# Optimization experiments

Hardware: AMD Instinct MI355X
Metric: run time of the kernel (lower is better)

The kernel has to match this reference:

```python
import jax, jax.numpy as jnp
import numpy as np

N_NODES = 100000
N_EDGES = 800000
VOCAB = 100
D_FEAT = 10
D = 64
EPS = 1e-8  # torch F.cosine_similarity eps


def setup_inputs() -> dict:
    key = jax.random.key(0)
    ks = jax.random.split(key, 8)
    return {
        "nodes": jax.random.randint(ks[0], (N_NODES,), 0, VOCAB),
        "edges": jax.random.randint(ks[1], (N_EDGES, 2), 0, N_NODES),
        "features": jax.random.normal(ks[2], (N_NODES, D_FEAT), dtype=jnp.float32),
        "node_emb": jax.random.normal(ks[3], (VOCAB, D), dtype=jnp.float32),
        "feat_W": jax.random.normal(ks[4], (D, D_FEAT), dtype=jnp.float32) * 0.1,
        "feat_b": jnp.zeros((D,), dtype=jnp.float32),
        "conv1_W": jax.random.normal(ks[5], (D, D), dtype=jnp.float32) * 0.1,
        "conv1_b": jnp.zeros((D,), dtype=jnp.float32),
        "pattern_emb": jax.random.normal(ks[6], (VOCAB, D), dtype=jnp.float32),
        "pattern_id": 42,  # hash(node_type) % 100
    }


def reference(nodes, edges, features, node_emb, feat_W, feat_b,
              conv1_W, conv1_b, pattern_emb, pattern_id):
    # initial embeddings: type embedding + linear feature projection  [N, D]
    embeds = node_emb[nodes] + (features @ feat_W.T + feat_b)

    src, dst = edges[:, 0], edges[:, 1]
    for _ in range(2):  # fixed 2 message-passing rounds (structural loop)
        # scatter-add messages from src to dst (order-independent sum)
        agg = jnp.zeros_like(embeds).at[dst].add(embeds[src])
        embeds = jax.nn.relu((embeds + agg) @ conv1_W.T + conv1_b)

    # cosine similarity of each node embedding against the pattern embedding
    p = pattern_emb[pattern_id]  # [D]
    num = embeds @ p  # [N]
    denom = jnp.maximum(jnp.linalg.norm(embeds, axis=1), EPS) * \
            jnp.maximum(jnp.linalg.norm(p), EPS)
    return num / denom  # [N] match scores
```

## Files before the change

kernel.cpp:

```cpp
#include <hip/hip_runtime.h>
#include <hip/hip_bf16.h>

#define N_NODES 100000
#define N_EDGES 800000
#define D 64
#define SCAN_B 256
#define NB1 ((N_NODES + SCAN_B - 1) / SCAN_B)
#define FILL_BLOCKS (N_EDGES / 256)
#define INIT_BLOCKS (N_NODES * D / 256)

__device__ __forceinline__ unsigned short f2bf(float f) {
    union { float f; unsigned u; } v; v.f = f;
    unsigned r = v.u + 0x7fffu + ((v.u >> 16) & 1u);
    return (unsigned short)(r >> 16);
}
__device__ __forceinline__ void acc_bf8(float acc[8], uint4 u) {
    acc[0] += __uint_as_float(u.x << 16);
    acc[1] += __uint_as_float(u.x & 0xffff0000u);
    acc[2] += __uint_as_float(u.y << 16);
    acc[3] += __uint_as_float(u.y & 0xffff0000u);
    acc[4] += __uint_as_float(u.z << 16);
    acc[5] += __uint_as_float(u.z & 0xffff0000u);
    acc[6] += __uint_as_float(u.w << 16);
    acc[7] += __uint_as_float(u.w & 0xffff0000u);
}

__global__ __launch_bounds__(256) void hist_rank_kernel(
        const int2* __restrict__ edges,
        int* __restrict__ deg,
        int* __restrict__ rank) {
    int t = blockIdx.x * 256 + threadIdx.x;
    int2 e = edges[t];
    rank[t] = atomicAdd(&deg[e.y], 1);
}

__global__ void scan1_kernel(const int* __restrict__ deg,
                             int* __restrict__ row_ptr,
                             int* __restrict__ bsum) {
    __shared__ int tmp[SCAN_B];
    int t = threadIdx.x;
    int i = blockIdx.x * SCAN_B + t;
    int v = (i < N_NODES) ? deg[i] : 0;
    tmp[t] = v;
    __syncthreads();
#pragma unroll
    for (int off = 1; off < SCAN_B; off <<= 1) {
        int a = (t >= off) ? tmp[t - off] : 0;
        __syncthreads();
        tmp[t] += a;
        __syncthreads();
    }
    if (i < N_NODES) row_ptr[i] = tmp[t] - v;
    if (t == SCAN_B - 1) bsum[blockIdx.x] = tmp[t];
}

__global__ void scan2_kernel(const int* __restrict__ bsum, int* __restrict__ boff) {
    __shared__ int tmp[512];
    int t = threadIdx.x;
    int v = (t < NB1) ? bsum[t] : 0;
    tmp[t] = v;
    __syncthreads();
#pragma unroll
    for (int off = 1; off < 512; off <<= 1) {
        int a = (t >= off) ? tmp[t - off] : 0;
        __syncthreads();
        tmp[t] += a;
        __syncthreads();
    }
    if (t < NB1) boff[t] = tmp[t] - v;
}

__global__ void scan3_kernel(int* __restrict__ row_ptr,
                             const int* __restrict__ boff) {
    int i = blockIdx.x * SCAN_B + threadIdx.x;
    if (i < N_NODES) row_ptr[i] += boff[i >> 8];
    if (i == 0) row_ptr[N_NODES] = N_EDGES;
}

__global__ __launch_bounds__(256) void fill_init_kernel(
        const int2* __restrict__ edges,
        const int* __restrict__ rank,
        const int* __restrict__ rowp,
        int* __restrict__ col,
        const int* __restrict__ nodes,
        const float* __restrict__ features,
        const float* __restrict__ node_emb,
        const float* __restrict__ feat_W,
        const float* __restrict__ feat_b,
        unsigned short* __restrict__ embeds) {
    if (blockIdx.x < FILL_BLOCKS) {
        int t = blockIdx.x * 256 + threadIdx.x;
        int2 e = edges[t];
        col[rowp[e.y] + rank[t]] = e.x;
    } else {
        int tid = (blockIdx.x - FILL_BLOCKS) * 256 + threadIdx.x;
        int node = tid >> 6;
        int d = tid & 63;
        float acc = feat_b[d];
        const float* f = features + (size_t)node * 10;
        const float* w = feat_W + (size_t)d * 10;
#pragma unroll
        for (int j = 0; j < 10; ++j) acc += f[j] * w[j];
        embeds[tid] = f2bf(node_emb[(size_t)nodes[node] * D + d] + acc);
    }
}

__global__ __launch_bounds__(256, 6) void gather_x_kernel(
        const unsigned short* __restrict__ emb_in,
        const int* __restrict__ rowp,
        const int* __restrict__ col,
        float* __restrict__ x_out) {
    int lane = threadIdx.x & 63;
    int wv   = threadIdx.x >> 6;
    int node = blockIdx.x * 4 + wv;
    int g = lane >> 3;
    int c = lane & 7;

    int start = rowp[node];
    int end   = rowp[node + 1];

    float acc[8];
#pragma unroll
    for (int j = 0; j < 8; ++j) acc[j] = 0.f;
    if (g == 0) {
        uint4 u = ((const uint4*)(emb_in + (size_t)node * D))[c];
        acc_bf8(acc, u);
    }

    for (int base = start; base < end; base += 32) {
        int nb = end - base; if (nb > 32) nb = 32;
        int idx = (lane < nb) ? col[base + lane] : 0;
#pragma unroll
        for (int r = 0; r < 4; ++r) {
            int s = r * 8 + g;
            int src = __shfl(idx, s, 64);
            if (s < nb) {
                uint4 u = ((const uint4*)(emb_in + (size_t)src * D))[c];
                acc_bf8(acc, u);
            }
        }
    }

#pragma unroll
    for (int m = 8; m <= 32; m <<= 1) {
#pragma unroll
        for (int j = 0; j < 8; ++j) acc[j] += __shfl_xor(acc[j], m, 64);
    }

    if (g == 0) {
        float4 a0 = make_float4(acc[0], acc[1], acc[2], acc[3]);
        float4 a1 = make_float4(acc[4], acc[5], acc[6], acc[7]);
        float4* o = (float4*)(x_out + (size_t)node * D);
        o[2 * c]     = a0;
        o[2 * c + 1] = a1;
    }
}

template <bool SCORE>
__global__ __launch_bounds__(256) void conv_kernel(
        const float* __restrict__ x,
        const float* __restrict__ W,
        const float* __restrict__ b,
        const float* __restrict__ pattern_emb,
        const int* __restrict__ pattern_id,
        unsigned short* __restrict__ emb_out,
        float* __restrict__ score_out) {
    __shared__ float4 xs[4][16];

    int lane = threadIdx.x & 63;
    int wv   = threadIdx.x >> 6;
    float bias = b[lane];

    float4 Wr[16];
    const float4* W4 = (const float4*)(W + (size_t)lane * D);
#pragma unroll
    for (int k = 0; k < 16; ++k) Wr[k] = W4[k];

    float p = 0.f, pnorm = 1.f;
    if (SCORE) {
        p = pattern_emb[(size_t)pattern_id[0] * D + lane];
        float pn = p * p;
#pragma unroll
        for (int m = 32; m > 0; m >>= 1) pn += __shfl_xor(pn, m, 64);
        pnorm = fmaxf(sqrtf(pn), 1e-8f);
    }

    const int n_chunks = N_NODES / 4;
    for (int chunk = blockIdx.x; chunk < n_chunks; chunk += gridDim.x) {
        int node = chunk * 4 + wv;
        if (lane < 16)
            xs[wv][lane] = ((const float4*)(x + (size_t)node * D))[lane];
        asm volatile("s_waitcnt vmcnt(0) lgkmcnt(0)" ::: "memory");
        float y = bias;
#pragma unroll
        for (int k = 0; k < 16; ++k) {
            float4 x4 = xs[wv][k];
            y += Wr[k].x * x4.x + Wr[k].y * x4.y + Wr[k].z * x4.z + Wr[k].w * x4.w;
        }
        y = fmaxf(y, 0.0f);
        if (!SCORE) {
            emb_out[(size_t)node * D + lane] = f2bf(y);
        } else {
            float dot = y * p;
            float n2  = y * y;
#pragma unroll
            for (int m = 32; m > 0; m >>= 1) {
                dot += __shfl_xor(dot, m, 64);
                n2  += __shfl_xor(n2, m, 64);
            }
            if (lane == 0)
                score_out[node] = dot / (fmaxf(sqrtf(n2), 1e-8f) * pnorm);
        }
    }
}

__global__ void init_embeds_kernel(const int* __restrict__ nodes,
                                   const float* __restrict__ features,
                                   const float* __restrict__ node_emb,
                                   const float* __restrict__ feat_W,
                                   const float* __restrict__ feat_b,
                                   float* __restrict__ embeds) {
    int tid = blockIdx.x * blockDim.x + threadIdx.x;
    if (tid >= N_NODES * D) return;
    int node = tid >> 6;
    int d = tid & 63;
    float acc = feat_b[d];
    const float* f = features + (size_t)node * 10;
    const float* w = feat_W + (size_t)d * 10;
#pragma unroll
    for (int j = 0; j < 10; ++j) acc += f[j] * w[j];
    embeds[tid] = node_emb[(size_t)nodes[node] * D + d] + acc;
}

__global__ void scatter_add_kernel(const int* __restrict__ edges,
                                   const float* __restrict__ embeds,
                                   float* __restrict__ agg) {
    int tid = blockIdx.x * blockDim.x + threadIdx.x;
    int edge = tid >> 6;
    int lane = tid & 63;
    if (edge >= N_EDGES) return;
    int src = edges[2 * edge + 0];
    int dst = edges[2 * edge + 1];
    atomicAdd(&agg[(size_t)dst * D + lane], embeds[(size_t)src * D + lane]);
}

__global__ void conv_inplace_kernel(const float* __restrict__ agg,
                                    const float* __restrict__ W,
                                    const float* __restrict__ b,
                                    float* __restrict__ embeds) {
    __shared__ float Ws[D * 65];
    __shared__ float xs[4][D];
    for (int i = threadIdx.x; i < D * D; i += blockDim.x) {
        int d = i >> 6, k = i & 63;
        Ws[d * 65 + k] = W[i];
    }
    __syncthreads();
    int lane_d = threadIdx.x & 63;
    int local_n = threadIdx.x >> 6;
    float bias = b[lane_d];
    const int n_chunks = (N_NODES + 3) / 4;
    for (int chunk = blockIdx.x; chunk < n_chunks; chunk += gridDim.x) {
        int node = chunk * 4 + local_n;
        if (node < N_NODES) {
            size_t base = (size_t)node * D + lane_d;
            xs[local_n][lane_d] = embeds[base] + agg[base];
        }
        __syncthreads();
        if (node < N_NODES) {
            float acc = bias;
#pragma unroll
            for (int k = 0; k < D; ++k) acc += xs[local_n][k] * Ws[lane_d * 65 + k];
            embeds[(size_t)node * D + lane_d] = fmaxf(acc, 0.0f);
        }
        __syncthreads();
    }
}

__global__ void final_score_kernel(const float* __restrict__ embeds,
                                   const float* __restrict__ pattern_emb,
                                   const int* __restrict__ pattern_id,
                                   float* __restrict__ out) {
    int lane = threadIdx.x & 63;
    int wave = threadIdx.x >> 6;
    int node = blockIdx.x * 4 + wave;
    int pid = pattern_id[0];
    float p = pattern_emb[(size_t)pid * D + lane];
    float pn = p * p;
#pragma unroll
    for (int m = 32; m > 0; m >>= 1) pn += __shfl_xor(pn, m, 64);
    if (node < N_NODES) {
        float e = embeds[(size_t)node * D + lane];
        float dot = e * p;
        float n2 = e * e;
#pragma unroll
        for (int m = 32; m > 0; m >>= 1) {
            dot += __shfl_xor(dot, m, 64);
            n2  += __shfl_xor(n2, m, 64);
        }
        if (lane == 0) {
            float denom = fmaxf(sqrtf(n2), 1e-8f) * fmaxf(sqrtf(pn), 1e-8f);
            out[node] = dot / denom;
        }
    }
}

extern "C" void kernel_launch(void* const* d_in, const int* in_sizes, int n_in,
                              void* d_out, int out_size, void* d_ws, size_t ws_size,
                              hipStream_t stream) {
    const int*   nodes       = (const int*)d_in[0];
    const int*   edges       = (const int*)d_in[1];
    const float* features    = (const float*)d_in[2];
    const float* node_emb    = (const float*)d_in[3];
    const float* feat_W      = (const float*)d_in[4];
    const float* feat_b      = (const float*)d_in[5];
    const float* conv1_W     = (const float*)d_in[6];
    const float* conv1_b     = (const float*)d_in[7];
    const float* pattern_emb = (const float*)d_in[8];
    const int*   pattern_id  = (const int*)d_in[9];
    float* out = (float*)d_out;

    const size_t emb_f32_bytes = (size_t)N_NODES * D * sizeof(float);
    const size_t emb_bf_bytes  = (size_t)N_NODES * D * 2;
    auto align256 = [](size_t x) { return (x + 255) & ~(size_t)255; };

    size_t o_embA = 0;
    size_t o_embB = o_embA + align256(emb_bf_bytes);
    size_t o_xbuf = o_embB + align256(emb_bf_bytes);
    size_t o_col  = o_xbuf + align256(emb_f32_bytes);
    size_t o_rank = o_col  + align256((size_t)N_EDGES * 4);
    size_t o_row  = o_rank + align256((size_t)N_EDGES * 4);
    size_t o_deg  = o_row  + align256((size_t)(N_NODES + 1) * 4);
    size_t o_bsum = o_deg  + align256((size_t)N_NODES * 4);
    size_t o_boff = o_bsum + align256((size_t)NB1 * 4);
    size_t need   = o_boff + align256((size_t)NB1 * 4);

    char* ws = (char*)d_ws;

    if (ws_size >= need) {
        unsigned short* embA = (unsigned short*)(ws + o_embA);
        unsigned short* embB = (unsigned short*)(ws + o_embB);
        float* xbuf = (float*)(ws + o_xbuf);
        int*   col  = (int*)(ws + o_col);
        int*   rank = (int*)(ws + o_rank);
        int*   rowp = (int*)(ws + o_row);
        int*   deg  = (int*)(ws + o_deg);
        int*   bsum = (int*)(ws + o_bsum);
        int*   boff = (int*)(ws + o_boff);

        hipMemsetAsync(deg, 0, (size_t)N_NODES * 4, stream);
        hist_rank_kernel<<<FILL_BLOCKS, 256, 0, stream>>>((const int2*)edges, deg, rank);
        scan1_kernel<<<NB1, SCAN_B, 0, stream>>>(deg, rowp, bsum);
        scan2_kernel<<<1, 512, 0, stream>>>(bsum, boff);
        scan3_kernel<<<NB1, SCAN_B, 0, stream>>>(rowp, boff);
        fill_init_kernel<<<FILL_BLOCKS + INIT_BLOCKS, 256, 0, stream>>>(
            (const int2*)edges, rank, rowp, col,
            nodes, features, node_emb, feat_W, feat_b, embA);

        gather_x_kernel<<<N_NODES / 4, 256, 0, stream>>>(embA, rowp, col, xbuf);
        conv_kernel<false><<<2048, 256, 0, stream>>>(
            xbuf, conv1_W, conv1_b, pattern_emb, pattern_id, embB, nullptr);
        gather_x_kernel<<<N_NODES / 4, 256, 0, stream>>>(embB, rowp, col, xbuf);
        conv_kernel<true><<<2048, 256, 0, stream>>>(
            xbuf, conv1_W, conv1_b, pattern_emb, pattern_id, nullptr, out);
    } else {
        float* embeds = (float*)ws;
        float* agg = (float*)(ws + align256(emb_f32_bytes));
        init_embeds_kernel<<<(N_NODES * D + 255) / 256, 256, 0, stream>>>(
            nodes, features, node_emb, feat_W, feat_b, embeds);
        for (int it = 0; it < 2; ++it) {
            hipMemsetAsync(agg, 0, emb_f32_bytes, stream);
            long long total = (long long)N_EDGES * 64;
            scatter_add_kernel<<<(int)((total + 255) / 256), 256, 0, stream>>>(edges, embeds, agg);
            conv_inplace_kernel<<<2048, 256, 0, stream>>>(agg, conv1_W, conv1_b, embeds);
        }
        final_score_kernel<<<(N_NODES + 3) / 4, 256, 0, stream>>>(
            embeds, pattern_emb, pattern_id, out);
    }
}
```

Baseline: 300.6 us.

## Replace per-node conv GEMV with 64-node shared-memory tiled GEMM

The dense conv step now processes 64 nodes per block as a small tiled GEMM. X and W are staged in padded shared memory and each thread computes a 4x4 output register tile. It drops the old grid-stride loop, where each wave held a full W row in registers and stalled on a full memory wait per node. Outputs are staged in shared memory for coalesced 16-byte bf16 stores, and the score path reduces each node's dot product and norm in one thread. This trades per-block W reloads and extra barriers for more arithmetic reuse and far more blocks in flight.

After: 259.7 us. 1.16x faster.

```diff
diff --git a/kernel.cpp b/kernel.cpp
--- a/kernel.cpp
+++ b/kernel.cpp
@@ -8,6 +8,9 @@
 #define NB1 ((N_NODES + SCAN_B - 1) / SCAN_B)
 #define FILL_BLOCKS (N_EDGES / 256)
 #define INIT_BLOCKS (N_NODES * D / 256)
+#define CT 64
+#define XS 68
+#define OS 72
 
 __device__ __forceinline__ unsigned short f2bf(float f) {
     union { float f; unsigned u; } v; v.f = f;
@@ -157,7 +160,7 @@
 }
 
 template <bool SCORE>
-__global__ __launch_bounds__(256) void conv_kernel(
+__global__ __launch_bounds__(256) void conv_tile_kernel(
         const float* __restrict__ x,
         const float* __restrict__ W,
         const float* __restrict__ b,
@@ -165,51 +168,86 @@
         const int* __restrict__ pattern_id,
         unsigned short* __restrict__ emb_out,
         float* __restrict__ score_out) {
-    __shared__ float4 xs[4][16];
-
-    int lane = threadIdx.x & 63;
-    int wv   = threadIdx.x >> 6;
-    float bias = b[lane];
-
-    float4 Wr[16];
-    const float4* W4 = (const float4*)(W + (size_t)lane * D);
-#pragma unroll
-    for (int k = 0; k < 16; ++k) Wr[k] = W4[k];
-
-    float p = 0.f, pnorm = 1.f;
-    if (SCORE) {
-        p = pattern_emb[(size_t)pattern_id[0] * D + lane];
-        float pn = p * p;
-#pragma unroll
-        for (int m = 32; m > 0; m >>= 1) pn += __shfl_xor(pn, m, 64);
-        pnorm = fmaxf(sqrtf(pn), 1e-8f);
-    }
-
-    const int n_chunks = N_NODES / 4;
-    for (int chunk = blockIdx.x; chunk < n_chunks; chunk += gridDim.x) {
-        int node = chunk * 4 + wv;
-        if (lane < 16)
-            xs[wv][lane] = ((const float4*)(x + (size_t)node * D))[lane];
-        asm volatile("s_waitcnt vmcnt(0) lgkmcnt(0)" ::: "memory");
-        float y = bias;
-#pragma unroll
-        for (int k = 0; k < 16; ++k) {
-            float4 x4 = xs[wv][k];
-            y += Wr[k].x * x4.x + Wr[k].y * x4.y + Wr[k].z * x4.z + Wr[k].w * x4.w;
-        }
-        y = fmaxf(y, 0.0f);
-        if (!SCORE) {
-            emb_out[(size_t)node * D + lane] = f2bf(y);
-        } else {
-            float dot = y * p;
-            float n2  = y * y;
-#pragma unroll
-            for (int m = 32; m > 0; m >>= 1) {
-                dot += __shfl_xor(dot, m, 64);
-                n2  += __shfl_xor(n2, m, 64);
+    __shared__ float Xs[CT][XS];
+    __shared__ float Wsh[D][XS];
+    __shared__ unsigned short Os[CT][OS];
+    __shared__ float ps[D];
+
+    int t = threadIdx.x;
+    int base = blockIdx.x * CT;
+    int i = t & 15;
+    int j = t >> 4;
+
+    float bj[4];
+#pragma unroll
+    for (int dj = 0; dj < 4; ++dj) bj[dj] = b[j + 16 * dj];
+
+    {
+        int c = t & 15;
+        int r0 = t >> 4;
+#pragma unroll
+        for (int p4 = 0; p4 < 4; ++p4) {
+            int r = r0 + p4 * 16;
+            float4 wv4 = ((const float4*)(W + (size_t)r * D))[c];
+            *((float4*)&Wsh[r][4 * c]) = wv4;
+            int node = base + r;
+            int nc = node < N_NODES ? node : (N_NODES - 1);
+            float4 xv4 = ((const float4*)(x + (size_t)nc * D))[c];
+            *((float4*)&Xs[r][4 * c]) = xv4;
+        }
+    }
+    if (SCORE && t < D) ps[t] = pattern_emb[(size_t)pattern_id[0] * D + t];
+    __syncthreads();
+
+    float acc[4][4] = {};
+    for (int k4 = 0; k4 < 16; ++k4) {
+        float4 xr[4], wr[4];
+#pragma unroll
+        for (int di = 0; di < 4; ++di) xr[di] = *((const float4*)&Xs[i + 16 * di][4 * k4]);
+#pragma unroll
+        for (int dj = 0; dj < 4; ++dj) wr[dj] = *((const float4*)&Wsh[j + 16 * dj][4 * k4]);
+#pragma unroll
+        for (int di = 0; di < 4; ++di)
+#pragma unroll
+            for (int dj = 0; dj < 4; ++dj)
+                acc[di][dj] += xr[di].x * wr[dj].x + xr[di].y * wr[dj].y
+                             + xr[di].z * wr[dj].z + xr[di].w * wr[dj].w;
+    }
+
+    if (!SCORE) {
+#pragma unroll
+        for (int di = 0; di < 4; ++di)
+#pragma unroll
+            for (int dj = 0; dj < 4; ++dj)
+                Os[i + 16 * di][j + 16 * dj] = f2bf(fmaxf(acc[di][dj] + bj[dj], 0.f));
+        __syncthreads();
+#pragma unroll
+        for (int q = 0; q < 2; ++q) {
+            int idx = t + q * 256;
+            int r = idx >> 3, seg = idx & 7;
+            int node = base + r;
+            if (node < N_NODES)
+                ((uint4*)(emb_out + (size_t)node * D))[seg] = *((const uint4*)&Os[r][8 * seg]);
+        }
+    } else {
+        __syncthreads();
+#pragma unroll
+        for (int di = 0; di < 4; ++di)
+#pragma unroll
+            for (int dj = 0; dj < 4; ++dj)
+                Xs[i + 16 * di][j + 16 * dj] = fmaxf(acc[di][dj] + bj[dj], 0.f);
+        __syncthreads();
+        if (t < CT) {
+            float dot = 0.f, n2 = 0.f, pn = 0.f;
+#pragma unroll 8
+            for (int k = 0; k < D; ++k) {
+                float yk = Xs[t][k];
+                float pk = ps[k];
+                dot += yk * pk; n2 += yk * yk; pn += pk * pk;
             }
-            if (lane == 0)
-                score_out[node] = dot / (fmaxf(sqrtf(n2), 1e-8f) * pnorm);
+            int node = base + t;
+            if (node < N_NODES)
+                score_out[node] = dot / (fmaxf(sqrtf(n2), 1e-8f) * fmaxf(sqrtf(pn), 1e-8f));
         }
     }
 }
@@ -356,11 +394,13 @@
             (const int2*)edges, rank, rowp, col,
             nodes, features, node_emb, feat_W, feat_b, embA);
 
+        const int conv_grid = (N_NODES + CT - 1) / CT;
+
         gather_x_kernel<<<N_NODES / 4, 256, 0, stream>>>(embA, rowp, col, xbuf);
-        conv_kernel<false><<<2048, 256, 0, stream>>>(
+        conv_tile_kernel<false><<<conv_grid, 256, 0, stream>>>(
             xbuf, conv1_W, conv1_b, pattern_emb, pattern_id, embB, nullptr);
         gather_x_kernel<<<N_NODES / 4, 256, 0, stream>>>(embB, rowp, col, xbuf);
-        conv_kernel<true><<<2048, 256, 0, stream>>>(
+        conv_tile_kernel<true><<<conv_grid, 256, 0, stream>>>(
             xbuf, conv1_W, conv1_b, pattern_emb, pattern_id, nullptr, out);
     } else {
         float* embeds = (float*)ws;
```
